# Performance work log

Measured on AMD Instinct MI355X. Metric: run time of the kernel, lower is better.

Reference implementation:

```python
import jax, jax.numpy as jnp
import numpy as np

DIM = 1024
N_HEADS = 16
HEAD_DIM = DIM // N_HEADS
EPS = 1e-05
ROPE_BASE = 1000000.0


def apply_rope(x, base=ROPE_BASE):
    # x: [b, seq, heads, head_dim]
    b, seq, n_heads, dim = x.shape
    half = dim // 2
    i = jnp.arange(half)
    theta = 1.0 / base ** (2 * i / dim)
    pos = jnp.arange(seq)
    angles = pos[:, None] * theta[None, :]            # [seq, half]
    cos = jnp.cos(angles)[None, :, None, :]           # [1, seq, 1, half]
    sin = jnp.sin(angles)[None, :, None, :]
    x1, x2 = jnp.split(x, 2, axis=-1)
    return jnp.concatenate([x1 * cos - x2 * sin, x1 * sin + x2 * cos], axis=-1)


def setup_inputs() -> dict:
    key = jax.random.key(0)
    ks = jax.random.split(key, 6)
    b, seq = 2, 2048
    scale = 1.0 / np.sqrt(DIM)
    x = jax.random.normal(ks[0], (b, seq, DIM), dtype=jnp.float32)
    w_norm = jnp.ones((DIM,), dtype=jnp.float32)
    Wq = jax.random.normal(ks[1], (DIM, DIM), dtype=jnp.float32) * scale
    Wk = jax.random.normal(ks[2], (DIM, DIM), dtype=jnp.float32) * scale
    Wv = jax.random.normal(ks[3], (DIM, DIM), dtype=jnp.float32) * scale
    Wo = jax.random.normal(ks[4], (DIM, DIM), dtype=jnp.float32) * scale
    return {"x": x, "w_norm": w_norm, "Wq": Wq, "Wk": Wk, "Wv": Wv, "Wo": Wo}


def reference(x, w_norm, Wq, Wk, Wv, Wo):
    b, seq, d = x.shape
    # RMSNorm
    rms = jnp.sqrt(jnp.mean(x * x, axis=-1, keepdims=True) + EPS)
    x_norm = x / rms * w_norm
    # QKV projections (Dense without bias: y = x @ W)
    q = (x_norm @ Wq).reshape(b, seq, N_HEADS, HEAD_DIM)
    k = (x_norm @ Wk).reshape(b, seq, N_HEADS, HEAD_DIM)
    v = (x_norm @ Wv).reshape(b, seq, N_HEADS, HEAD_DIM)
    q = apply_rope(q)
    k = apply_rope(k)
    # Causal attention with full [b,h,t,s] scores (faithful to source)
    scores = jnp.einsum('bthd,bshd->bhts', q, k) / jnp.sqrt(jnp.float32(HEAD_DIM))
    causal = jnp.triu(jnp.full((seq, seq), -jnp.inf, dtype=scores.dtype), k=1)
    scores = scores + causal[None, None, :, :]
    attn = jax.nn.softmax(scores, axis=-1)
    out = jnp.einsum('bhts,bshd->bthd', attn, v).reshape(b, seq, d)
    return out @ Wo
```

## Files before the change

### kernel.cpp

```cpp
#include <hip/hip_runtime.h>

#define DIM 1024
#define SEQ 2048
#define BATCH 2
#define NHEADS 16
#define HD 64
#define ROWS (BATCH * SEQ)

typedef __bf16 bf16x8 __attribute__((ext_vector_type(8)));
typedef __bf16 bf16x4 __attribute__((ext_vector_type(4)));
typedef float f32x4 __attribute__((ext_vector_type(4)));
typedef float f32x16 __attribute__((ext_vector_type(16)));
typedef unsigned u32x4 __attribute__((ext_vector_type(4)));

__device__ __forceinline__ f32x4 f4zero() {
    f32x4 z = {0.f, 0.f, 0.f, 0.f};
    return z;
}

__device__ __forceinline__ unsigned cvtpk(float lo, float hi) {
    unsigned r;
    asm("v_cvt_pk_bf16_f32 %0, %1, %2" : "=v"(r) : "v"(lo), "v"(hi));
    return r;
}

__device__ __forceinline__ void pl32swap(unsigned& a, unsigned& b) {
    asm volatile("v_permlane32_swap_b32 %0, %1" : "+v"(a), "+v"(b));
}

__device__ __forceinline__ int slot_base(int qp) {
    if (qp < 16) return qp;
    if (qp < 32) return 16 + 2 * (qp - 16);
    if (qp < 48) return 48 + 3 * (qp - 32);
    return 96 + 4 * (qp - 48);
}

#define GLOAD_LDS16(g, l)                                                                  \
    __builtin_amdgcn_global_load_lds((const __attribute__((address_space(1))) void*)(g),   \
                                     (__attribute__((address_space(3))) void*)(l), 16, 0, 0)

__global__ __launch_bounds__(256) void rmsnorm_bf16(const float* __restrict__ x,
                                                    const float* __restrict__ w,
                                                    __bf16* __restrict__ xn) {
    int row = blockIdx.x;
    int t = threadIdx.x;
    float4 v = ((const float4*)(x + (size_t)row * DIM))[t];
    float ss = v.x * v.x + v.y * v.y + v.z * v.z + v.w * v.w;
#pragma unroll
    for (int off = 1; off < 64; off <<= 1) ss += __shfl_xor(ss, off);
    __shared__ float red[4];
    if ((t & 63) == 0) red[t >> 6] = ss;
    __syncthreads();
    ss = red[0] + red[1] + red[2] + red[3];
    float scale = rsqrtf(ss * (1.0f / DIM) + 1e-5f);
    float4 wv = ((const float4*)w)[t];
    bf16x4 o;
    o[0] = (__bf16)(v.x * scale * wv.x);
    o[1] = (__bf16)(v.y * scale * wv.y);
    o[2] = (__bf16)(v.z * scale * wv.z);
    o[3] = (__bf16)(v.w * scale * wv.w);
    *(bf16x4*)(xn + (size_t)row * DIM + t * 4) = o;
}

__global__ __launch_bounds__(256) void wcvt_kernel(const float* __restrict__ Wq,
                                                   const float* __restrict__ Wk,
                                                   const float* __restrict__ Wv,
                                                   const float* __restrict__ Wo,
                                                   __bf16* tq, __bf16* tk, __bf16* tv, __bf16* to_) {
    int z = blockIdx.z;
    const float* W = z == 0 ? Wq : z == 1 ? Wk : z == 2 ? Wv : Wo;
    __bf16* T = z == 0 ? tq : z == 1 ? tk : z == 2 ? tv : to_;
    __shared__ float tile[32][33];
    int n0 = blockIdx.x * 32, k0 = blockIdx.y * 32;
    int tx = threadIdx.x & 31, ty = threadIdx.x >> 5;
#pragma unroll
    for (int j = 0; j < 32; j += 8) tile[ty + j][tx] = W[(size_t)(k0 + ty + j) * DIM + n0 + tx];
    __syncthreads();
#pragma unroll
    for (int j = 0; j < 32; j += 8)
        T[(size_t)(n0 + ty + j) * DIM + k0 + tx] = (__bf16)tile[tx][ty + j];
}

__global__ __launch_bounds__(256) void rope_table_kernel(float* __restrict__ cosT,
                                                         float* __restrict__ sinT) {
    int idx = blockIdx.x * 256 + threadIdx.x;
    int s = idx >> 5, i = idx & 31;
    float e = (2.0f * (float)i) / 64.0f;
    float theta = 1.0f / powf(1000000.0f, e);
    float ang = (float)s * theta;
    cosT[idx] = cosf(ang);
    sinT[idx] = sinf(ang);
}

__device__ __forceinline__ void gemm_core(const __bf16* __restrict__ A,
                                          const __bf16* __restrict__ Bt,
                                          int K, __bf16* As, __bf16* Bs,
                                          f32x4 (&acc)[4][4], int row0, int col0) {
    int tid = threadIdx.x;
    int w = tid >> 6, l = tid & 63, l15 = l & 15, g = l >> 4;
    int wr = (w >> 1) << 6, wc = (w & 1) << 6;

    int sr0 = tid >> 2;
    int sr1 = 64 + (tid >> 2);
    int lc0 = (((tid & 3) ^ ((tid >> 3) & 3)) << 3);
    const __bf16* gA0 = A + (size_t)(row0 + sr0) * K + lc0;
    const __bf16* gA1 = A + (size_t)(row0 + sr1) * K + lc0;
    const __bf16* gB0 = Bt + (size_t)(col0 + sr0) * K + lc0;
    const __bf16* gB1 = Bt + (size_t)(col0 + sr1) * K + lc0;
    __bf16* lA0 = As + w * 512;
    __bf16* lA1 = As + 2048 + w * 512;
    __bf16* lB0 = Bs + w * 512;
    __bf16* lB1 = Bs + 2048 + w * 512;

    int rca = ((g ^ ((l15 >> 1) & 3)) << 3);

#pragma unroll
    for (int i = 0; i < 4; ++i)
#pragma unroll
        for (int j = 0; j < 4; ++j) acc[i][j] = f4zero();

    for (int k0 = 0; k0 < K; k0 += 32) {
        __syncthreads();
        GLOAD_LDS16(gA0 + k0, lA0);
        GLOAD_LDS16(gA1 + k0, lA1);
        GLOAD_LDS16(gB0 + k0, lB0);
        GLOAD_LDS16(gB1 + k0, lB1);
        __syncthreads();

        bf16x8 af[4], bfr[4];
#pragma unroll
        for (int i = 0; i < 4; ++i) af[i] = *(const bf16x8*)&As[(wr + i * 16 + l15) * 32 + rca];
#pragma unroll
        for (int j = 0; j < 4; ++j) bfr[j] = *(const bf16x8*)&Bs[(wc + j * 16 + l15) * 32 + rca];
        __builtin_amdgcn_s_setprio(1);
#pragma unroll
        for (int i = 0; i < 4; ++i)
#pragma unroll
            for (int j = 0; j < 4; ++j)
                acc[i][j] = __builtin_amdgcn_mfma_f32_16x16x32_bf16(af[i], bfr[j], acc[i][j], 0, 0, 0);
        __builtin_amdgcn_s_setprio(0);
    }
}

__global__ __launch_bounds__(256) void gemm_qkv_kernel(const __bf16* __restrict__ xn,
                                                       const __bf16* __restrict__ wq,
                                                       const __bf16* __restrict__ wk,
                                                       const __bf16* __restrict__ wv,
                                                       __bf16* __restrict__ qo,
                                                       __bf16* __restrict__ ko,
                                                       __bf16* __restrict__ vt,
                                                       const float* __restrict__ cosT,
                                                       const float* __restrict__ sinT) {
    __shared__ __bf16 As[128 * 32];
    __shared__ __bf16 Bs[128 * 32];
    int bid = blockIdx.x;
    int tid = threadIdx.x;
    int w = tid >> 6, l = tid & 63, l15 = l & 15, g = l >> 4;
    int wr = (w >> 1) << 6, wc = (w & 1) << 6;
    f32x4 acc[4][4];

    if (bid < 512) {
        int z = bid >> 8, t = bid & 255;
        int col0 = (t & 7) << 7, row0 = (t >> 3) << 7;
        gemm_core(xn, z ? wk : wq, DIM, As, Bs, acc, row0, col0);
        __bf16* C = z ? ko : qo;
        int colbase = col0 + wc;
#pragma unroll
        for (int i = 0; i < 4; ++i) {
#pragma unroll
            for (int r = 0; r < 4; ++r) {
                int row = row0 + wr + i * 16 + g * 4 + r;
                int s = row & (SEQ - 1);
#pragma unroll
                for (int j = 0; j < 2; ++j) {
                    float c = cosT[s * 32 + j * 16 + l15];
                    float sn = sinT[s * 32 + j * 16 + l15];
                    float x1 = acc[i][j][r], x2 = acc[i][j + 2][r];
                    C[(size_t)row * DIM + colbase + j * 16 + l15] = (__bf16)(x1 * c - x2 * sn);
                    C[(size_t)row * DIM + colbase + (j + 2) * 16 + l15] = (__bf16)(x1 * sn + x2 * c);
                }
            }
        }
    } else {
        int t = bid - 512;
        int b = t >> 7, r7 = t & 127;
        int row0 = (r7 >> 4) << 7;
        int col0 = (r7 & 15) << 7;
        gemm_core(wv, xn + (size_t)b * SEQ * DIM, DIM, As, Bs, acc, row0, col0);
        __bf16* C = vt + (size_t)b * (NHEADS * HD) * SEQ;
#pragma unroll
        for (int i = 0; i < 4; ++i)
#pragma unroll
            for (int j = 0; j < 4; ++j)
#pragma unroll
                for (int r = 0; r < 4; ++r) {
                    int row = row0 + wr + i * 16 + g * 4 + r;
                    int col = col0 + wc + j * 16 + l15;
                    C[(size_t)row * SEQ + col] = (__bf16)acc[i][j][r];
                }
    }
}

__global__ __launch_bounds__(256) void gemm_out_kernel(const __bf16* __restrict__ ctx,
                                                       const __bf16* __restrict__ wo,
                                                       float* __restrict__ out) {
    __shared__ __bf16 As[128 * 32];
    __shared__ __bf16 Bs[128 * 32];
    int row0 = (int)blockIdx.y << 7, col0 = (int)blockIdx.x << 7;
    f32x4 acc[4][4];
    gemm_core(ctx, wo, DIM, As, Bs, acc, row0, col0);
    int tid = threadIdx.x;
    int w = tid >> 6, l = tid & 63, l15 = l & 15, g = l >> 4;
    int wr = (w >> 1) << 6, wc = (w & 1) << 6;
#pragma unroll
    for (int i = 0; i < 4; ++i)
#pragma unroll
        for (int j = 0; j < 4; ++j)
#pragma unroll
            for (int r = 0; r < 4; ++r) {
                int row = row0 + wr + i * 16 + g * 4 + r;
                int col = col0 + wc + j * 16 + l15;
                out[(size_t)row * DIM + col] = acc[i][j][r];
            }
}

__global__ __launch_bounds__(64, 3) void attn_mfma_kernel(const __bf16* __restrict__ q,
                                                          const __bf16* __restrict__ k,
                                                          const __bf16* __restrict__ vt,
                                                          __bf16* __restrict__ part_O,
                                                          float* __restrict__ part_ml) {
    int bh = blockIdx.x;
    int slot = 159 - (int)blockIdx.y;
    int qp, ci;
    if (slot < 16) { qp = slot; ci = 0; }
    else if (slot < 48) { int t = slot - 16; qp = 16 + (t >> 1); ci = t & 1; }
    else if (slot < 96) { int t = slot - 48; qp = 32 + t / 3; ci = t - 3 * (t / 3); }
    else { int t = slot - 96; qp = 48 + (t >> 2); ci = t & 3; }
    int local = qp - (ci << 4);
    int ntiles = local < 16 ? local + 1 : 16;
    int dtile = local < 16 ? local : -1;
    int ks0 = ci << 9;

    int b = bh >> 4, h = bh & 15;
    int l = threadIdx.x & 63;
    int l31 = l & 31, hi = l >> 5;
    size_t hoff = (size_t)(b * SEQ) * DIM + h * HD;
    const __bf16* vth = vt + (size_t)bh * HD * SEQ;
    int qrow = qp * 32 + l31;

    bf16x8 qf[4];
    {
        const __bf16* qptr = q + hoff + (size_t)qrow * DIM + hi * 8;
        const float c2 = 0.125f * 1.44269504f;
#pragma unroll
        for (int g = 0; g < 4; ++g) {
            bf16x8 t0 = *(const bf16x8*)(qptr + g * 16);
#pragma unroll
            for (int e = 0; e < 8; ++e) qf[g][e] = (__bf16)((float)t0[e] * c2);
        }
    }

    f32x16 oA, oB;
#pragma unroll
    for (int r = 0; r < 16; ++r) {
        oA[r] = 0.f;
        oB[r] = 0.f;
    }
    float m_run = -1e30f, l_run = 0.f;

    const __bf16* kptr = k + hoff + (size_t)(ks0 + l31) * DIM + hi * 8;
    const __bf16* vptr0 = vth + (size_t)l31 * SEQ + ks0 + hi * 8;
    const __bf16* vptr1 = vth + (size_t)(32 + l31) * SEQ + ks0 + hi * 8;

    bf16x8 ka[4], kb[4];
#pragma unroll
    for (int g = 0; g < 4; ++g) ka[g] = *(const bf16x8*)(kptr + g * 16);
    kptr += 32 * DIM;

    auto tile_body = [&](bf16x8 (&kcur)[4], bf16x8 (&knxt)[4], int st) {
        if (st + 1 < ntiles) {
#pragma unroll
            for (int g = 0; g < 4; ++g) knxt[g] = *(const bf16x8*)(kptr + g * 16);
            kptr += 32 * DIM;
        }
        bf16x8 vv0 = *(const bf16x8*)(vptr0);
        bf16x8 vv1 = *(const bf16x8*)(vptr0 + 16);
        bf16x8 vv2 = *(const bf16x8*)(vptr1);
        bf16x8 vv3 = *(const bf16x8*)(vptr1 + 16);
        vptr0 += 32;
        vptr1 += 32;

        f32x16 sa;
#pragma unroll
        for (int r = 0; r < 16; ++r) sa[r] = 0.f;
        __builtin_amdgcn_s_setprio(1);
#pragma unroll
        for (int g = 0; g < 4; ++g)
            sa = __builtin_amdgcn_mfma_f32_32x32x16_bf16(kcur[g], qf[g], sa, 0, 0, 0);
        __builtin_amdgcn_s_setprio(0);

        if (st == dtile) {
            int s0 = ks0 + (st << 5);
#pragma unroll
            for (int r = 0; r < 16; ++r) {
                int kg = s0 + (r & 3) + 8 * (r >> 2) + 4 * hi;
                if (kg > qrow) sa[r] = -1e30f;
            }
        }

        float lmax = sa[0];
#pragma unroll
        for (int r = 1; r < 16; ++r) lmax = fmaxf(lmax, sa[r]);
        if (!__all(lmax <= m_run + 10.0f)) {
            float omax = fmaxf(lmax, __shfl_xor(lmax, 32));
            float m_new = fmaxf(m_run, omax);
            float alpha = exp2f(m_run - m_new);
            l_run *= alpha;
#pragma unroll
            for (int r = 0; r < 16; ++r) {
                oA[r] *= alpha;
                oB[r] *= alpha;
            }
            m_run = m_new;
        }
        float ls = 0.f;
#pragma unroll
        for (int r = 0; r < 16; ++r) {
            sa[r] = exp2f(sa[r] - m_run);
            ls += sa[r];
        }
        l_run += ls + __shfl_xor(ls, 32);

        unsigned a0 = cvtpk(sa[0], sa[1]), b0 = cvtpk(sa[4], sa[5]);
        pl32swap(a0, b0);
        unsigned c0 = cvtpk(sa[2], sa[3]), d0 = cvtpk(sa[6], sa[7]);
        pl32swap(c0, d0);
        u32x4 t0 = {a0, c0, b0, d0};
        bf16x8 pa0 = __builtin_bit_cast(bf16x8, t0);
        unsigned a1 = cvtpk(sa[8], sa[9]), b1 = cvtpk(sa[12], sa[13]);
        pl32swap(a1, b1);
        unsigned c1 = cvtpk(sa[10], sa[11]), d1 = cvtpk(sa[14], sa[15]);
        pl32swap(c1, d1);
        u32x4 t1 = {a1, c1, b1, d1};
        bf16x8 pa1 = __builtin_bit_cast(bf16x8, t1);

        __builtin_amdgcn_s_setprio(1);
        oA = __builtin_amdgcn_mfma_f32_32x32x16_bf16(vv0, pa0, oA, 0, 0, 0);
        oA = __builtin_amdgcn_mfma_f32_32x32x16_bf16(vv1, pa1, oA, 0, 0, 0);
        oB = __builtin_amdgcn_mfma_f32_32x32x16_bf16(vv2, pa0, oB, 0, 0, 0);
        oB = __builtin_amdgcn_mfma_f32_32x32x16_bf16(vv3, pa1, oB, 0, 0, 0);
        __builtin_amdgcn_s_setprio(0);
    };

    int st = 0;
    while (st < ntiles) {
        tile_body(ka, kb, st);
        ++st;
        if (st >= ntiles) break;
        tile_body(kb, ka, st);
        ++st;
    }

    int gslot = bh * 160 + slot;
    __bf16* po = part_O + (size_t)gslot * 2048 + l31 * 64;
#pragma unroll
    for (int rr = 0; rr < 16; rr += 4) {
        int d0 = 8 * (rr >> 2) + 4 * hi;
        uint2 pA = {cvtpk(oA[rr], oA[rr + 1]), cvtpk(oA[rr + 2], oA[rr + 3])};
        uint2 pB = {cvtpk(oB[rr], oB[rr + 1]), cvtpk(oB[rr + 2], oB[rr + 3])};
        *(uint2*)&po[d0] = pA;
        *(uint2*)&po[32 + d0] = pB;
    }
    if (hi == 0) {
        part_ml[(size_t)gslot * 64 + l31] = m_run;
        part_ml[(size_t)gslot * 64 + 32 + l31] = l_run;
    }
}

__global__ __launch_bounds__(128) void attn_combine_kernel(const __bf16* __restrict__ part_O,
                                                           const float* __restrict__ part_ml,
                                                           __bf16* __restrict__ ctx) {
    int bh = blockIdx.x, qp = blockIdx.y;
    int b = bh >> 4, h = bh & 15;
    int nch = (qp >> 4) + 1;
    int base = slot_base(qp);
    size_t so = (size_t)bh * 160 + base;
    int t = threadIdx.x;
    int row = t >> 2, dseg = (t & 3) << 4;

    float mv0 = -1e30f, mv1 = -1e30f, mv2 = -1e30f, mv3 = -1e30f;
    mv0 = part_ml[(so + 0) * 64 + row];
    if (nch > 1) mv1 = part_ml[(so + 1) * 64 + row];
    if (nch > 2) mv2 = part_ml[(so + 2) * 64 + row];
    if (nch > 3) mv3 = part_ml[(so + 3) * 64 + row];
    float mmax = fmaxf(fmaxf(mv0, mv1), fmaxf(mv2, mv3));

    float acc[16];
#pragma unroll
    for (int e = 0; e < 16; ++e) acc[e] = 0.f;
    float lsum = 0.f;

#pragma unroll 4
    for (int i = 0; i < 4; ++i) {
        if (i >= nch) break;
        float mi = i == 0 ? mv0 : i == 1 ? mv1 : i == 2 ? mv2 : mv3;
        float wsc = exp2f(mi - mmax);
        lsum += wsc * part_ml[(so + i) * 64 + 32 + row];
        const __bf16* po = part_O + (so + i) * 2048 + row * 64 + dseg;
        bf16x8 a = *(const bf16x8*)po;
        bf16x8 b2 = *(const bf16x8*)(po + 8);
#pragma unroll
        for (int e = 0; e < 8; ++e) {
            acc[e] += wsc * (float)a[e];
            acc[8 + e] += wsc * (float)b2[e];
        }
    }

    float inv = 1.0f / lsum;
    bf16x8 oa, ob;
#pragma unroll
    for (int e = 0; e < 8; ++e) {
        oa[e] = (__bf16)(acc[e] * inv);
        ob[e] = (__bf16)(acc[8 + e] * inv);
    }
    size_t off = ((size_t)(b * SEQ) + qp * 32 + row) * DIM + h * HD + dseg;
    *(bf16x8*)&ctx[off] = oa;
    *(bf16x8*)&ctx[off + 8] = ob;
}

extern "C" void kernel_launch(void* const* d_in, const int* in_sizes, int n_in,
                              void* d_out, int out_size, void* d_ws, size_t ws_size,
                              hipStream_t stream) {
    const float* x = (const float*)d_in[0];
    const float* w_norm = (const float*)d_in[1];
    const float* Wq = (const float*)d_in[2];
    const float* Wk = (const float*)d_in[3];
    const float* Wv = (const float*)d_in[4];
    const float* Wo = (const float*)d_in[5];
    float* out = (float*)d_out;
    char* w8 = (char*)d_ws;

    const size_t MB = 1ull << 20;
    __bf16* xn = (__bf16*)(w8);
    __bf16* wtq = (__bf16*)(w8 + 8 * MB);
    __bf16* wtk = (__bf16*)(w8 + 10 * MB);
    __bf16* wtv = (__bf16*)(w8 + 12 * MB);
    __bf16* part_O = (__bf16*)(w8);
    __bf16* wto = (__bf16*)(w8 + 20 * MB);
    __bf16* qb = (__bf16*)(w8 + 22 * MB);
    __bf16* kb = (__bf16*)(w8 + 30 * MB);
    __bf16* vtb = (__bf16*)(w8 + 38 * MB);
    __bf16* ctx = (__bf16*)(w8 + 46 * MB);
    float* cosT = (float*)(w8 + 54 * MB);
    float* sinT = cosT + SEQ * 32;
    float* part_ml = (float*)(w8 + 55 * MB);

    wcvt_kernel<<<dim3(32, 32, 4), 256, 0, stream>>>(Wq, Wk, Wv, Wo, wtq, wtk, wtv, wto);
    rmsnorm_bf16<<<ROWS, 256, 0, stream>>>(x, w_norm, xn);
    rope_table_kernel<<<(SEQ * 32) / 256, 256, 0, stream>>>(cosT, sinT);

    gemm_qkv_kernel<<<768, 256, 0, stream>>>(xn, wtq, wtk, wtv, qb, kb, vtb, cosT, sinT);

    attn_mfma_kernel<<<dim3(BATCH * NHEADS, 160), 64, 0, stream>>>(qb, kb, vtb, part_O, part_ml);
    attn_combine_kernel<<<dim3(BATCH * NHEADS, SEQ / 32), 128, 0, stream>>>(part_O, part_ml, ctx);

    gemm_out_kernel<<<dim3(DIM / 128, ROWS / 128), 256, 0, stream>>>(ctx, wto, out);
}
```

Measured before the change: 159.5 us.

## Store Q/K/V in MFMA fragment layout and repartition attention into 4-wave blocks

The QKV GEMM epilogue now writes Q, K and V in a per-head, per-32-row-tile layout that matches the MFMA operand fragments, so each attention lane loads contiguous 16-byte chunks instead of strided rows. Attention work is split into 96 slots per head with at most two key chunks (instead of up to four across 160 slots), and four waves are packed into each 256-thread block. The combine kernel is simplified to merge at most two partials. It also uses raw v_exp_f32 and tree-style max/sum reductions; the epilogue now does scattered 2-byte stores and the longer chunks may reduce parallelism balance.

```diff
diff --git a/kernel.cpp b/kernel.cpp
--- a/kernel.cpp
+++ b/kernel.cpp
@@ -28,11 +28,10 @@
     asm volatile("v_permlane32_swap_b32 %0, %1" : "+v"(a), "+v"(b));
 }
 
-__device__ __forceinline__ int slot_base(int qp) {
-    if (qp < 16) return qp;
-    if (qp < 32) return 16 + 2 * (qp - 16);
-    if (qp < 48) return 48 + 3 * (qp - 32);
-    return 96 + 4 * (qp - 48);
+__device__ __forceinline__ float fexp2(float x) {
+    float r;
+    asm("v_exp_f32 %0, %1" : "=v"(r) : "v"(x));
+    return r;
 }
 
 #define GLOAD_LDS16(g, l)                                                                  \
@@ -146,16 +145,16 @@
                                                        const __bf16* __restrict__ wq,
                                                        const __bf16* __restrict__ wk,
                                                        const __bf16* __restrict__ wv,
-                                                       __bf16* __restrict__ qo,
-                                                       __bf16* __restrict__ ko,
-                                                       __bf16* __restrict__ vt,
+                                                       __bf16* __restrict__ qf,
+                                                       __bf16* __restrict__ kf,
+                                                       __bf16* __restrict__ vf,
                                                        const float* __restrict__ cosT,
                                                        const float* __restrict__ sinT) {
     __shared__ __bf16 As[128 * 32];
     __shared__ __bf16 Bs[128 * 32];
     int bid = blockIdx.x;
     int tid = threadIdx.x;
-    int w = tid >> 6, l = tid & 63, l15 = l & 15, g = l >> 4;
+    int w = tid >> 6, l = tid & 63, l15 = l & 15, gq = l >> 4;
     int wr = (w >> 1) << 6, wc = (w & 1) << 6;
     f32x4 acc[4][4];
 
@@ -163,21 +162,31 @@
         int z = bid >> 8, t = bid & 255;
         int col0 = (t & 7) << 7, row0 = (t >> 3) << 7;
         gemm_core(xn, z ? wk : wq, DIM, As, Bs, acc, row0, col0);
-        __bf16* C = z ? ko : qo;
+        __bf16* F = z ? kf : qf;
         int colbase = col0 + wc;
 #pragma unroll
         for (int i = 0; i < 4; ++i) {
 #pragma unroll
             for (int r = 0; r < 4; ++r) {
-                int row = row0 + wr + i * 16 + g * 4 + r;
+                int row = row0 + wr + i * 16 + gq * 4 + r;
                 int s = row & (SEQ - 1);
+                int bb = row >> 11;
 #pragma unroll
                 for (int j = 0; j < 2; ++j) {
                     float c = cosT[s * 32 + j * 16 + l15];
                     float sn = sinT[s * 32 + j * 16 + l15];
                     float x1 = acc[i][j][r], x2 = acc[i][j + 2][r];
-                    C[(size_t)row * DIM + colbase + j * 16 + l15] = (__bf16)(x1 * c - x2 * sn);
-                    C[(size_t)row * DIM + colbase + (j + 2) * 16 + l15] = (__bf16)(x1 * sn + x2 * c);
+#pragma unroll
+                    for (int p = 0; p < 2; ++p) {
+                        int col = colbase + (j + 2 * p) * 16 + l15;
+                        float v = p ? (x1 * sn + x2 * c) : (x1 * c - x2 * sn);
+                        int hh = col >> 6, dd = col & 63;
+                        size_t tb = (size_t)(bb * 16 + hh) * 64 + (s >> 5);
+                        tb = tb * 4 + ((dd >> 4) & 3);
+                        int lane = (s & 31) | (((dd >> 3) & 1) << 5);
+                        size_t idx = (tb * 64 + lane) * 8 + (dd & 7);
+                        F[idx] = (__bf16)v;
+                    }
                 }
             }
         }
@@ -187,17 +196,24 @@
         int row0 = (r7 >> 4) << 7;
         int col0 = (r7 & 15) << 7;
         gemm_core(wv, xn + (size_t)b * SEQ * DIM, DIM, As, Bs, acc, row0, col0);
-        __bf16* C = vt + (size_t)b * (NHEADS * HD) * SEQ;
-#pragma unroll
-        for (int i = 0; i < 4; ++i)
-#pragma unroll
-            for (int j = 0; j < 4; ++j)
-#pragma unroll
-                for (int r = 0; r < 4; ++r) {
-                    int row = row0 + wr + i * 16 + g * 4 + r;
+#pragma unroll
+        for (int i = 0; i < 4; ++i) {
+#pragma unroll
+            for (int r = 0; r < 4; ++r) {
+                int rowN = row0 + wr + i * 16 + gq * 4 + r;
+                int hh = rowN >> 6, dd = rowN & 63;
+#pragma unroll
+                for (int j = 0; j < 4; ++j) {
                     int col = col0 + wc + j * 16 + l15;
-                    C[(size_t)row * SEQ + col] = (__bf16)acc[i][j][r];
+                    size_t tb = (size_t)(b * 16 + hh) * 64 + (col >> 5);
+                    tb = tb * 2 + (dd >> 5);
+                    tb = tb * 2 + ((col >> 4) & 1);
+                    int lane = (dd & 31) | (((col >> 3) & 1) << 5);
+                    size_t idx = (tb * 64 + lane) * 8 + (col & 7);
+                    vf[idx] = (__bf16)acc[i][j][r];
                 }
+            }
+        }
     }
 }
 
@@ -224,41 +240,46 @@
             }
 }
 
-__global__ __launch_bounds__(64, 3) void attn_mfma_kernel(const __bf16* __restrict__ q,
-                                                          const __bf16* __restrict__ k,
-                                                          const __bf16* __restrict__ vt,
-                                                          __bf16* __restrict__ part_O,
-                                                          float* __restrict__ part_ml) {
+__global__ __launch_bounds__(256, 3) void attn_mfma_kernel(const __bf16* __restrict__ qf,
+                                                           const __bf16* __restrict__ kf,
+                                                           const __bf16* __restrict__ vf,
+                                                           __bf16* __restrict__ part_O,
+                                                           float* __restrict__ part_ml) {
     int bh = blockIdx.x;
-    int slot = 159 - (int)blockIdx.y;
+    int tid = threadIdx.x, wvx = tid >> 6, l = tid & 63;
+    int wslot = (int)blockIdx.y * 4 + wvx;
+    int slot = 95 - wslot;
     int qp, ci;
-    if (slot < 16) { qp = slot; ci = 0; }
-    else if (slot < 48) { int t = slot - 16; qp = 16 + (t >> 1); ci = t & 1; }
-    else if (slot < 96) { int t = slot - 48; qp = 32 + t / 3; ci = t - 3 * (t / 3); }
-    else { int t = slot - 96; qp = 48 + (t >> 2); ci = t & 3; }
-    int local = qp - (ci << 4);
-    int ntiles = local < 16 ? local + 1 : 16;
-    int dtile = local < 16 ? local : -1;
-    int ks0 = ci << 9;
-
-    int b = bh >> 4, h = bh & 15;
-    int l = threadIdx.x & 63;
+    if (slot < 32) {
+        qp = slot;
+        ci = 0;
+    } else {
+        int t = slot - 32;
+        qp = 32 + (t >> 1);
+        ci = t & 1;
+    }
+    int rem = qp - (ci << 5);
+    int ntiles = rem < 32 ? rem + 1 : 32;
+    int dtile = rem < 32 ? rem : -1;
+    int t0 = ci << 5;
+
     int l31 = l & 31, hi = l >> 5;
-    size_t hoff = (size_t)(b * SEQ) * DIM + h * HD;
-    const __bf16* vth = vt + (size_t)bh * HD * SEQ;
     int qrow = qp * 32 + l31;
 
-    bf16x8 qf[4];
+    bf16x8 qfr[4];
     {
-        const __bf16* qptr = q + hoff + (size_t)qrow * DIM + hi * 8;
+        const __bf16* qp_ = qf + ((size_t)bh * 64 + qp) * 2048 + (size_t)l * 8;
         const float c2 = 0.125f * 1.44269504f;
 #pragma unroll
         for (int g = 0; g < 4; ++g) {
-            bf16x8 t0 = *(const bf16x8*)(qptr + g * 16);
-#pragma unroll
-            for (int e = 0; e < 8; ++e) qf[g][e] = (__bf16)((float)t0[e] * c2);
-        }
-    }
+            bf16x8 tq = *(const bf16x8*)(qp_ + g * 512);
+#pragma unroll
+            for (int e = 0; e < 8; ++e) qfr[g][e] = (__bf16)((float)tq[e] * c2);
+        }
+    }
+
+    const __bf16* kfp = kf + ((size_t)bh * 64 + t0) * 2048 + (size_t)l * 8;
+    const __bf16* vfp = vf + ((size_t)bh * 64 + t0) * 2048 + (size_t)l * 8;
 
     f32x16 oA, oB;
 #pragma unroll
@@ -268,27 +289,21 @@
     }
     float m_run = -1e30f, l_run = 0.f;
 
-    const __bf16* kptr = k + hoff + (size_t)(ks0 + l31) * DIM + hi * 8;
-    const __bf16* vptr0 = vth + (size_t)l31 * SEQ + ks0 + hi * 8;
-    const __bf16* vptr1 = vth + (size_t)(32 + l31) * SEQ + ks0 + hi * 8;
-
     bf16x8 ka[4], kb[4];
 #pragma unroll
-    for (int g = 0; g < 4; ++g) ka[g] = *(const bf16x8*)(kptr + g * 16);
-    kptr += 32 * DIM;
+    for (int g = 0; g < 4; ++g) ka[g] = *(const bf16x8*)(kfp + g * 512);
 
     auto tile_body = [&](bf16x8 (&kcur)[4], bf16x8 (&knxt)[4], int st) {
         if (st + 1 < ntiles) {
-#pragma unroll
-            for (int g = 0; g < 4; ++g) knxt[g] = *(const bf16x8*)(kptr + g * 16);
-            kptr += 32 * DIM;
-        }
-        bf16x8 vv0 = *(const bf16x8*)(vptr0);
-        bf16x8 vv1 = *(const bf16x8*)(vptr0 + 16);
-        bf16x8 vv2 = *(const bf16x8*)(vptr1);
-        bf16x8 vv3 = *(const bf16x8*)(vptr1 + 16);
-        vptr0 += 32;
-        vptr1 += 32;
+            const __bf16* kn = kfp + (size_t)(st + 1) * 2048;
+#pragma unroll
+            for (int g = 0; g < 4; ++g) knxt[g] = *(const bf16x8*)(kn + g * 512);
+        }
+        const __bf16* vp = vfp + (size_t)st * 2048;
+        bf16x8 v00 = *(const bf16x8*)(vp);
+        bf16x8 v01 = *(const bf16x8*)(vp + 512);
+        bf16x8 v10 = *(const bf16x8*)(vp + 1024);
+        bf16x8 v11 = *(const bf16x8*)(vp + 1536);
 
         f32x16 sa;
 #pragma unroll
@@ -296,11 +311,11 @@
         __builtin_amdgcn_s_setprio(1);
 #pragma unroll
         for (int g = 0; g < 4; ++g)
-            sa = __builtin_amdgcn_mfma_f32_32x32x16_bf16(kcur[g], qf[g], sa, 0, 0, 0);
+            sa = __builtin_amdgcn_mfma_f32_32x32x16_bf16(kcur[g], qfr[g], sa, 0, 0, 0);
         __builtin_amdgcn_s_setprio(0);
 
         if (st == dtile) {
-            int s0 = ks0 + (st << 5);
+            int s0 = (t0 + st) << 5;
 #pragma unroll
             for (int r = 0; r < 16; ++r) {
                 int kg = s0 + (r & 3) + 8 * (r >> 2) + 4 * hi;
@@ -308,13 +323,16 @@
             }
         }
 
-        float lmax = sa[0];
-#pragma unroll
-        for (int r = 1; r < 16; ++r) lmax = fmaxf(lmax, sa[r]);
+        float mx[8];
+#pragma unroll
+        for (int r = 0; r < 8; ++r) mx[r] = fmaxf(sa[r], sa[r + 8]);
+#pragma unroll
+        for (int r = 0; r < 4; ++r) mx[r] = fmaxf(mx[r], mx[r + 4]);
+        float lmax = fmaxf(fmaxf(mx[0], mx[1]), fmaxf(mx[2], mx[3]));
         if (!__all(lmax <= m_run + 10.0f)) {
             float omax = fmaxf(lmax, __shfl_xor(lmax, 32));
             float m_new = fmaxf(m_run, omax);
-            float alpha = exp2f(m_run - m_new);
+            float alpha = fexp2(m_run - m_new);
             l_run *= alpha;
 #pragma unroll
             for (int r = 0; r < 16; ++r) {
@@ -323,32 +341,34 @@
             }
             m_run = m_new;
         }
-        float ls = 0.f;
-#pragma unroll
-        for (int r = 0; r < 16; ++r) {
-            sa[r] = exp2f(sa[r] - m_run);
-            ls += sa[r];
-        }
+#pragma unroll
+        for (int r = 0; r < 16; ++r) sa[r] = fexp2(sa[r] - m_run);
+        float s8[8];
+#pragma unroll
+        for (int r = 0; r < 8; ++r) s8[r] = sa[r] + sa[r + 8];
+#pragma unroll
+        for (int r = 0; r < 4; ++r) s8[r] += s8[r + 4];
+        float ls = (s8[0] + s8[1]) + (s8[2] + s8[3]);
         l_run += ls + __shfl_xor(ls, 32);
 
         unsigned a0 = cvtpk(sa[0], sa[1]), b0 = cvtpk(sa[4], sa[5]);
         pl32swap(a0, b0);
         unsigned c0 = cvtpk(sa[2], sa[3]), d0 = cvtpk(sa[6], sa[7]);
         pl32swap(c0, d0);
-        u32x4 t0 = {a0, c0, b0, d0};
-        bf16x8 pa0 = __builtin_bit_cast(bf16x8, t0);
+        u32x4 t4a = {a0, c0, b0, d0};
+        bf16x8 pa0 = __builtin_bit_cast(bf16x8, t4a);
         unsigned a1 = cvtpk(sa[8], sa[9]), b1 = cvtpk(sa[12], sa[13]);
         pl32swap(a1, b1);
         unsigned c1 = cvtpk(sa[10], sa[11]), d1 = cvtpk(sa[14], sa[15]);
         pl32swap(c1, d1);
-        u32x4 t1 = {a1, c1, b1, d1};
-        bf16x8 pa1 = __builtin_bit_cast(bf16x8, t1);
+        u32x4 t4b = {a1, c1, b1, d1};
+        bf16x8 pa1 = __builtin_bit_cast(bf16x8, t4b);
 
         __builtin_amdgcn_s_setprio(1);
-        oA = __builtin_amdgcn_mfma_f32_32x32x16_bf16(vv0, pa0, oA, 0, 0, 0);
-        oA = __builtin_amdgcn_mfma_f32_32x32x16_bf16(vv1, pa1, oA, 0, 0, 0);
-        oB = __builtin_amdgcn_mfma_f32_32x32x16_bf16(vv2, pa0, oB, 0, 0, 0);
-        oB = __builtin_amdgcn_mfma_f32_32x32x16_bf16(vv3, pa1, oB, 0, 0, 0);
+        oA = __builtin_amdgcn_mfma_f32_32x32x16_bf16(v00, pa0, oA, 0, 0, 0);
+        oA = __builtin_amdgcn_mfma_f32_32x32x16_bf16(v01, pa1, oA, 0, 0, 0);
+        oB = __builtin_amdgcn_mfma_f32_32x32x16_bf16(v10, pa0, oB, 0, 0, 0);
+        oB = __builtin_amdgcn_mfma_f32_32x32x16_bf16(v11, pa1, oB, 0, 0, 0);
         __builtin_amdgcn_s_setprio(0);
     };
 
@@ -361,7 +381,7 @@
         ++st;
     }
 
-    int gslot = bh * 160 + slot;
+    int gslot = bh * 96 + slot;
     __bf16* po = part_O + (size_t)gslot * 2048 + l31 * 64;
 #pragma unroll
     for (int rr = 0; rr < 16; rr += 4) {
@@ -382,29 +402,27 @@
                                                            __bf16* __restrict__ ctx) {
     int bh = blockIdx.x, qp = blockIdx.y;
     int b = bh >> 4, h = bh & 15;
-    int nch = (qp >> 4) + 1;
-    int base = slot_base(qp);
-    size_t so = (size_t)bh * 160 + base;
+    int nch = 1 + (qp >> 5);
+    int base = qp < 32 ? qp : 32 + 2 * (qp - 32);
+    size_t so = (size_t)bh * 96 + base;
     int t = threadIdx.x;
     int row = t >> 2, dseg = (t & 3) << 4;
 
-    float mv0 = -1e30f, mv1 = -1e30f, mv2 = -1e30f, mv3 = -1e30f;
-    mv0 = part_ml[(so + 0) * 64 + row];
+    float mv0 = part_ml[so * 64 + row];
+    float mv1 = -1e30f;
     if (nch > 1) mv1 = part_ml[(so + 1) * 64 + row];
-    if (nch > 2) mv2 = part_ml[(so + 2) * 64 + row];
-    if (nch > 3) mv3 = part_ml[(so + 3) * 64 + row];
-    float mmax = fmaxf(fmaxf(mv0, mv1), fmaxf(mv2, mv3));
+    float mmax = fmaxf(mv0, mv1);
 
     float acc[16];
 #pragma unroll
     for (int e = 0; e < 16; ++e) acc[e] = 0.f;
     float lsum = 0.f;
 
-#pragma unroll 4
-    for (int i = 0; i < 4; ++i) {
+#pragma unroll 2
+    for (int i = 0; i < 2; ++i) {
         if (i >= nch) break;
-        float mi = i == 0 ? mv0 : i == 1 ? mv1 : i == 2 ? mv2 : mv3;
-        float wsc = exp2f(mi - mmax);
+        float mi = i == 0 ? mv0 : mv1;
+        float wsc = fexp2(mi - mmax);
         lsum += wsc * part_ml[(so + i) * 64 + 32 + row];
         const __bf16* po = part_O + (so + i) * 2048 + row * 64 + dseg;
         bf16x8 a = *(const bf16x8*)po;
@@ -446,22 +464,22 @@
     __bf16* wtk = (__bf16*)(w8 + 10 * MB);
     __bf16* wtv = (__bf16*)(w8 + 12 * MB);
     __bf16* part_O = (__bf16*)(w8);
-    __bf16* wto = (__bf16*)(w8 + 20 * MB);
-    __bf16* qb = (__bf16*)(w8 + 22 * MB);
-    __bf16* kb = (__bf16*)(w8 + 30 * MB);
-    __bf16* vtb = (__bf16*)(w8 + 38 * MB);
-    __bf16* ctx = (__bf16*)(w8 + 46 * MB);
-    float* cosT = (float*)(w8 + 54 * MB);
+    float* part_ml = (float*)(w8 + 12 * MB);
+    __bf16* wto = (__bf16*)(w8 + 14 * MB);
+    __bf16* qf = (__bf16*)(w8 + 16 * MB);
+    __bf16* kf = (__bf16*)(w8 + 24 * MB);
+    __bf16* vf = (__bf16*)(w8 + 32 * MB);
+    __bf16* ctx = (__bf16*)(w8 + 40 * MB);
+    float* cosT = (float*)(w8 + 48 * MB);
     float* sinT = cosT + SEQ * 32;
-    float* part_ml = (float*)(w8 + 55 * MB);
 
     wcvt_kernel<<<dim3(32, 32, 4), 256, 0, stream>>>(Wq, Wk, Wv, Wo, wtq, wtk, wtv, wto);
     rmsnorm_bf16<<<ROWS, 256, 0, stream>>>(x, w_norm, xn);
     rope_table_kernel<<<(SEQ * 32) / 256, 256, 0, stream>>>(cosT, sinT);
 
-    gemm_qkv_kernel<<<768, 256, 0, stream>>>(xn, wtq, wtk, wtv, qb, kb, vtb, cosT, sinT);
-
-    attn_mfma_kernel<<<dim3(BATCH * NHEADS, 160), 64, 0, stream>>>(qb, kb, vtb, part_O, part_ml);
+    gemm_qkv_kernel<<<768, 256, 0, stream>>>(xn, wtq, wtk, wtv, qf, kf, vf, cosT, sinT);
+
+    attn_mfma_kernel<<<dim3(BATCH * NHEADS, 24), 256, 0, stream>>>(qf, kf, vf, part_O, part_ml);
     attn_combine_kernel<<<dim3(BATCH * NHEADS, SEQ / 32), 128, 0, stream>>>(part_O, part_ml, ctx);
 
     gemm_out_kernel<<<dim3(DIM / 128, ROWS / 128), 256, 0, stream>>>(ctx, wto, out);
```

Measured after the change: 140.9 us. 11.7% less time.
